# Optimization experiments

Measured on AMD Instinct MI355X. Metric: run time of the kernel, lower is better.

The kernel has to match this reference:

```python
import jax, jax.numpy as jnp
import numpy as np

B, S, D, H, F = 4, 2048, 1024, 16, 4096
BS = 64               # sparse attention block size
DH = D // H           # head dim
EPS = 1e-5


def _layer_norm(x, g, b):
    m = jnp.mean(x, axis=-1, keepdims=True)
    v = jnp.mean(jnp.square(x - m), axis=-1, keepdims=True)
    return (x - m) * jax.lax.rsqrt(v + EPS) * g + b


def setup_inputs() -> dict:
    key = jax.random.key(0)
    ks = jax.random.split(key, 12)
    sc = 0.02
    return {
        "hidden_states": jax.random.normal(ks[0], (B, S, D), dtype=jnp.float32),
        "ln1_g": jnp.ones((D,), jnp.float32), "ln1_b": jnp.zeros((D,), jnp.float32),
        "ln2_g": jnp.ones((D,), jnp.float32), "ln2_b": jnp.zeros((D,), jnp.float32),
        "wq": jax.random.normal(ks[1], (D, D), jnp.float32) * sc, "bq": jnp.zeros((D,), jnp.float32),
        "wk": jax.random.normal(ks[2], (D, D), jnp.float32) * sc, "bk": jnp.zeros((D,), jnp.float32),
        "wv": jax.random.normal(ks[3], (D, D), jnp.float32) * sc, "bv": jnp.zeros((D,), jnp.float32),
        "wo": jax.random.normal(ks[4], (D, D), jnp.float32) * sc, "bo": jnp.zeros((D,), jnp.float32),
        "w1": jax.random.normal(ks[5], (D, F), jnp.float32) * sc, "b1": jnp.zeros((F,), jnp.float32),
        "w2": jax.random.normal(ks[6], (F, D), jnp.float32) * sc, "b2": jnp.zeros((D,), jnp.float32),
    }


def _heads(x, w, b):
    # [B,S,D] -> [B,H,S/BS,BS,DH] block layout
    y = (x @ w + b).reshape(B, S, H, DH).transpose(0, 2, 1, 3)
    return y.reshape(B, H, S // BS, BS, DH)


def _block_attention(x, wq, bq, wk, bk, wv, bv, wo, bo):
    q = _heads(x, wq, bq)
    k = _heads(x, wk, bk)
    v = _heads(x, wv, bv)
    scores = jnp.einsum("bhnqd,bhnkd->bhnqk", q, k) / jnp.sqrt(jnp.float32(DH))
    w = jax.nn.softmax(scores, axis=-1)           # block-local (sparse) attention weights
    o = jnp.einsum("bhnqk,bhnkd->bhnqd", w, v)
    o = o.reshape(B, H, S, DH).transpose(0, 2, 1, 3).reshape(B, S, D)
    return o @ wo + bo, w


def reference(hidden_states, ln1_g, ln1_b, ln2_g, ln2_b,
              wq, bq, wk, bk, wv, bv, wo, bo, w1, b1, w2, b2):
    # pre-norm attention + residual
    x1 = _layer_norm(hidden_states, ln1_g, ln1_b)
    attn_out, attn_w = _block_attention(x1, wq, bq, wk, bk, wv, bv, wo, bo)
    h = hidden_states + attn_out
    # pre-norm FFN + residual (exact GELU, matching torch nn.GELU default)
    x2 = _layer_norm(h, ln2_g, ln2_b)
    ff = jax.nn.gelu(x2 @ w1 + b1, approximate=False) @ w2 + b2
    return h + ff, attn_w
```

## Files before the change

kernel.cpp:

```cpp
#include <hip/hip_runtime.h>
#include <hip/hip_bf16.h>
#include <cmath>

using bf16 = __hip_bfloat16;
typedef __attribute__((ext_vector_type(8))) short short8;
typedef __attribute__((ext_vector_type(4))) float f32x4;

#define LDK 72

__device__ __forceinline__ float bf2f(bf16 v){ return __bfloat162float(v); }
__device__ __forceinline__ bf16 f2bf(float v){ return __float2bfloat16(v); }

__device__ __forceinline__ void ld16(const void* g, void* l) {
    __builtin_amdgcn_global_load_lds(
        (const __attribute__((address_space(1))) void*)g,
        (__attribute__((address_space(3))) void*)l, 16, 0, 0);
}

__device__ __forceinline__ float gelu_f(float x) {
    float u = 0.7978845608028654f * x * (1.0f + 0.044715f * x * x);
    float e = __expf(2.0f * u);
    float t = 1.0f - 2.0f / (e + 1.0f);
    return 0.5f * x * (1.0f + t);
}

__global__ __launch_bounds__(256) void transpose_f32_bf16(
    const float* __restrict__ in, bf16* __restrict__ out, int R, int C)
{
    __shared__ __align__(16) bf16 tile[64][72];
    const int c0 = blockIdx.x * 64, r0 = blockIdx.y * 64;
    const int t = threadIdx.x;
    const int lr = t >> 3, lc = (t & 7) * 8;
    for (int p = 0; p < 2; ++p) {
        int r = p * 32 + lr;
        const float* src = in + (size_t)(r0 + r) * C + c0 + lc;
        float4 a = *(const float4*)src;
        float4 b = *(const float4*)(src + 4);
        tile[r][lc + 0] = f2bf(a.x); tile[r][lc + 1] = f2bf(a.y);
        tile[r][lc + 2] = f2bf(a.z); tile[r][lc + 3] = f2bf(a.w);
        tile[r][lc + 4] = f2bf(b.x); tile[r][lc + 5] = f2bf(b.y);
        tile[r][lc + 6] = f2bf(b.z); tile[r][lc + 7] = f2bf(b.w);
    }
    __syncthreads();
    for (int p = 0; p < 2; ++p) {
        int r = p * 32 + lr;
        short8 v;
        for (int j = 0; j < 8; ++j) v[j] = *(const short*)&tile[lc + j][r];
        *(short8*)(out + (size_t)(c0 + r) * R + r0 + lc) = v;
    }
}

__global__ __launch_bounds__(256) void concat_bias(
    const float* __restrict__ bq, const float* __restrict__ bk,
    const float* __restrict__ bv, float* __restrict__ out)
{
    int i = blockIdx.x * 256 + threadIdx.x;
    const float* src = (i < 1024) ? bq : ((i < 2048) ? bk : bv);
    out[i] = src[i & 1023];
}

__global__ __launch_bounds__(256) void layernorm_k(
    const float* __restrict__ x, const float* __restrict__ g,
    const float* __restrict__ bta, bf16* __restrict__ out)
{
    const int row = blockIdx.x, t = threadIdx.x;
    const float* xr = x + (size_t)row * 1024;
    float v[4], s1 = 0.f, s2 = 0.f;
    for (int j = 0; j < 4; ++j) {
        float f = xr[j * 256 + t];
        v[j] = f; s1 += f; s2 += f * f;
    }
    for (int d = 1; d < 64; d <<= 1) { s1 += __shfl_xor(s1, d); s2 += __shfl_xor(s2, d); }
    __shared__ float red[2][4];
    int wave = t >> 6, lane = t & 63;
    if (lane == 0) { red[0][wave] = s1; red[1][wave] = s2; }
    __syncthreads();
    s1 = red[0][0] + red[0][1] + red[0][2] + red[0][3];
    s2 = red[1][0] + red[1][1] + red[1][2] + red[1][3];
    float mean = s1 * (1.0f / 1024.0f);
    float var  = s2 * (1.0f / 1024.0f) - mean * mean;
    float rs   = rsqrtf(var + 1e-5f);
    bf16* orow = out + (size_t)row * 1024;
    for (int j = 0; j < 4; ++j) {
        int c = j * 256 + t;
        orow[c] = f2bf((v[j] - mean) * rs * g[c] + bta[c]);
    }
}

template <int MODE, int TM>
__global__ __launch_bounds__(256) void gemm_bt(
    const bf16* __restrict__ A, const bf16* __restrict__ Bt,
    const float* __restrict__ bias, const float* __restrict__ res,
    void* __restrict__ C, int M, int N, int K)
{
    constexpr int MI = TM / 32;
    __shared__ __align__(16) bf16 As0[TM * 64];
    __shared__ __align__(16) bf16 Bs0[128 * 64];
    __shared__ __align__(16) bf16 As1[TM * 64];
    __shared__ __align__(16) bf16 Bs1[128 * 64];
    const int m0 = blockIdx.x * TM, n0 = blockIdx.y * 128;
    const int t = threadIdx.x;
    const int wave = t >> 6, lane = t & 63, lhi = lane >> 4, llo = lane & 15;
    const int wm = (wave & 1) * (TM / 2), wn = (wave >> 1) * 64;
    const int lrow = lane >> 3;
    const int lcolsw = ((lane & 7) ^ lrow) * 8;

    const bf16* Ag = A  + (size_t)(m0 + lrow) * K + lcolsw;
    const bf16* Bg = Bt + (size_t)(n0 + lrow) * K + lcolsw;

    f32x4 acc[MI][4];
    for (int i = 0; i < MI; ++i)
        for (int j = 0; j < 4; ++j) acc[i][j] = (f32x4){0.f, 0.f, 0.f, 0.f};

    auto issue = [&](int k0, bf16* As, bf16* Bs) {
        for (int p = 0; p < TM / 32; ++p) {
            int rb = wave * (TM / 4) + p * 8;
            ld16(Ag + (size_t)rb * K + k0, &As[rb * 64]);
        }
        for (int p = 0; p < 4; ++p) {
            int rb = wave * 32 + p * 8;
            ld16(Bg + (size_t)rb * K + k0, &Bs[rb * 64]);
        }
    };
    auto compute = [&](const bf16* As, const bf16* Bs) {
        for (int kk = 0; kk < 64; kk += 32) {
            const int gb = kk >> 3;
            short8 af[MI], bfr[4];
            for (int i = 0; i < MI; ++i) {
                int row = wm + i * 16 + llo;
                af[i] = *(const short8*)&As[row * 64 + (((gb + lhi) ^ (llo & 7)) * 8)];
            }
            for (int i = 0; i < 4; ++i) {
                int row = wn + i * 16 + llo;
                bfr[i] = *(const short8*)&Bs[row * 64 + (((gb + lhi) ^ (llo & 7)) * 8)];
            }
            for (int mi = 0; mi < MI; ++mi)
                for (int ni = 0; ni < 4; ++ni)
                    acc[mi][ni] = __builtin_amdgcn_mfma_f32_16x16x32_bf16(
                        af[mi], bfr[ni], acc[mi][ni], 0, 0, 0);
        }
    };

    issue(0, As0, Bs0);
    for (int k0 = 0; k0 < K; k0 += 128) {
        __syncthreads();
        issue(k0 + 64, As1, Bs1);
        compute(As0, Bs0);
        __syncthreads();
        if (k0 + 128 < K) issue(k0 + 128, As0, Bs0);
        compute(As1, Bs1);
    }

    for (int mi = 0; mi < MI; ++mi)
        for (int ni = 0; ni < 4; ++ni) {
            int row = m0 + wm + mi * 16 + lhi * 4;
            int col = n0 + wn + ni * 16 + llo;
            float bcol = bias[col];
            for (int r = 0; r < 4; ++r) {
                size_t idx = (size_t)(row + r) * N + col;
                float v = acc[mi][ni][r] + bcol;
                if (MODE == 0) {
                    ((bf16*)C)[idx] = f2bf(v);
                } else if (MODE == 1) {
                    ((float*)C)[idx] = v + res[idx];
                } else if (MODE == 2) {
                    ((bf16*)C)[idx] = f2bf(gelu_f(v));
                } else {
                    ((float*)C)[idx] = v + res[idx];
                }
            }
        }
}

__global__ __launch_bounds__(256) void attn_kernel(
    const bf16* __restrict__ qkv, float* __restrict__ attw, bf16* __restrict__ o)
{
    __shared__ __align__(16) bf16 qs[64][LDK];
    __shared__ __align__(16) bf16 ks[64][LDK];
    __shared__ __align__(16) bf16 vs[64][LDK];
    const int gid = blockIdx.x;
    const int blk = gid & 31, h = (gid >> 5) & 15, b = gid >> 9;
    const int t = threadIdx.x, wave = t >> 6, lane = t & 63;
    const int lhi = lane >> 4, llo = lane & 15;
    const int srow = t >> 3, scol = (t & 7) * 8;

    for (int p = 0; p < 2; ++p) {
        int r = p * 32 + srow;
        const bf16* base = qkv + (size_t)(b * 2048 + blk * 64 + r) * 3072 + h * 64 + scol;
        *(short8*)&qs[r][scol] = *(const short8*)(base);
        *(short8*)&ks[r][scol] = *(const short8*)(base + 1024);
        *(short8*)&vs[r][scol] = *(const short8*)(base + 2048);
    }
    __syncthreads();

    f32x4 sacc[4];
    for (int j = 0; j < 4; ++j) sacc[j] = (f32x4){0.f, 0.f, 0.f, 0.f};
    for (int kk = 0; kk < 64; kk += 32) {
        short8 aq = *(const short8*)&qs[wave * 16 + llo][kk + lhi * 8];
        for (int j = 0; j < 4; ++j) {
            short8 bk = *(const short8*)&ks[j * 16 + llo][kk + lhi * 8];
            sacc[j] = __builtin_amdgcn_mfma_f32_16x16x32_bf16(aq, bk, sacc[j], 0, 0, 0);
        }
    }
    float inv[4];
    for (int r = 0; r < 4; ++r) {
        float m = -1e30f;
        for (int j = 0; j < 4; ++j) m = fmaxf(m, sacc[j][r]);
        for (int d = 1; d < 16; d <<= 1) m = fmaxf(m, __shfl_xor(m, d));
        float s = 0.f;
        for (int j = 0; j < 4; ++j) {
            float e = expf((sacc[j][r] - m) * 0.125f);
            sacc[j][r] = e; s += e;
        }
        for (int d = 1; d < 16; d <<= 1) s += __shfl_xor(s, d);
        inv[r] = 1.0f / s;
    }
    __syncthreads();
    const size_t wbase = (size_t)gid * 4096;
    for (int j = 0; j < 4; ++j)
        for (int r = 0; r < 4; ++r) {
            int row = wave * 16 + lhi * 4 + r, col = j * 16 + llo;
            float pw = sacc[j][r] * inv[r];
            qs[row][col] = f2bf(pw);
            attw[wbase + row * 64 + col] = pw;
        }
    __syncthreads();

    f32x4 oacc[4];
    for (int nt = 0; nt < 4; ++nt) oacc[nt] = (f32x4){0.f, 0.f, 0.f, 0.f};
    for (int kk = 0; kk < 64; kk += 32) {
        short8 aw = *(const short8*)&qs[wave * 16 + llo][kk + lhi * 8];
        for (int nt = 0; nt < 4; ++nt) {
            short8 bv;
            for (int jj = 0; jj < 8; ++jj)
                bv[jj] = *(const short*)&vs[kk + lhi * 8 + jj][nt * 16 + llo];
            oacc[nt] = __builtin_amdgcn_mfma_f32_16x16x32_bf16(aw, bv, oacc[nt], 0, 0, 0);
        }
    }
    for (int nt = 0; nt < 4; ++nt)
        for (int r = 0; r < 4; ++r) {
            int row = wave * 16 + lhi * 4 + r, col = nt * 16 + llo;
            o[(size_t)(b * 2048 + blk * 64 + row) * 1024 + h * 64 + col] = f2bf(oacc[nt][r]);
        }
}

extern "C" void kernel_launch(void* const* d_in, const int* in_sizes, int n_in,
                              void* d_out, int out_size, void* d_ws, size_t ws_size,
                              hipStream_t stream)
{
    const float* hidden = (const float*)d_in[0];
    const float* ln1_g  = (const float*)d_in[1];
    const float* ln1_b  = (const float*)d_in[2];
    const float* ln2_g  = (const float*)d_in[3];
    const float* ln2_b  = (const float*)d_in[4];
    const float* wq = (const float*)d_in[5];  const float* bq = (const float*)d_in[6];
    const float* wk = (const float*)d_in[7];  const float* bk = (const float*)d_in[8];
    const float* wv = (const float*)d_in[9];  const float* bv = (const float*)d_in[10];
    const float* wo = (const float*)d_in[11]; const float* bo = (const float*)d_in[12];
    const float* w1 = (const float*)d_in[13]; const float* b1 = (const float*)d_in[14];
    const float* w2 = (const float*)d_in[15]; const float* b2 = (const float*)d_in[16];

    char* ws = (char*)d_ws;
    const size_t MB = 1u << 20;
    bf16*  wqkvT   = (bf16*)(ws +  0 * MB);
    bf16*  woT     = (bf16*)(ws +  6 * MB);
    bf16*  w1T     = (bf16*)(ws +  8 * MB);
    bf16*  w2T     = (bf16*)(ws + 16 * MB);
    float* biasQKV = (float*)(ws + 24 * MB);
    bf16*  x       = (bf16*)(ws + 25 * MB);
    bf16*  qkv     = (bf16*)(ws + 41 * MB);
    float* hbuf    = (float*)(ws + 41 * MB);
    bf16*  ffc     = (bf16*)(ws + 73 * MB);
    bf16*  obuf    = (bf16*)(ws + 89 * MB);

    float* out0 = (float*)d_out;
    float* attw = (float*)d_out + (size_t)8192 * 1024;

    transpose_f32_bf16<<<dim3(16, 16), 256, 0, stream>>>(wq, wqkvT,                 1024, 1024);
    transpose_f32_bf16<<<dim3(16, 16), 256, 0, stream>>>(wk, wqkvT + 1024 * 1024,   1024, 1024);
    transpose_f32_bf16<<<dim3(16, 16), 256, 0, stream>>>(wv, wqkvT + 2*1024*1024,   1024, 1024);
    transpose_f32_bf16<<<dim3(16, 16), 256, 0, stream>>>(wo, woT, 1024, 1024);
    transpose_f32_bf16<<<dim3(64, 16), 256, 0, stream>>>(w1, w1T, 1024, 4096);
    transpose_f32_bf16<<<dim3(16, 64), 256, 0, stream>>>(w2, w2T, 4096, 1024);
    concat_bias<<<12, 256, 0, stream>>>(bq, bk, bv, biasQKV);

    layernorm_k<<<8192, 256, 0, stream>>>(hidden, ln1_g, ln1_b, x);

    gemm_bt<0, 128><<<dim3(64, 24), 256, 0, stream>>>(x, wqkvT, biasQKV, nullptr, qkv,
                                                      8192, 3072, 1024);

    attn_kernel<<<2048, 256, 0, stream>>>(qkv, attw, obuf);

    gemm_bt<1, 64><<<dim3(128, 8), 256, 0, stream>>>(obuf, woT, bo, hidden, hbuf,
                                                     8192, 1024, 1024);

    layernorm_k<<<8192, 256, 0, stream>>>(hbuf, ln2_g, ln2_b, x);

    gemm_bt<2, 128><<<dim3(64, 32), 256, 0, stream>>>(x, w1T, b1, nullptr, ffc,
                                                      8192, 4096, 1024);

    gemm_bt<3, 64><<<dim3(128, 8), 256, 0, stream>>>(ffc, w2T, b2, hbuf, out0,
                                                     8192, 1024, 4096);
}
```

Measured before the change: 472.3 us.

## Halve GEMM K-tile to 32, reswizzle LDS, raise occupancy via launch bounds

The GEMM's shared-memory stage drops from 64 to 32 along K, which halves LDS use per block and lets more blocks fit on a CU. Launch bounds now request 3 or 4 blocks per CU depending on tile height. The LDS layout switches to a new 4-group XOR swizzle, and the fragment offsets are computed once before the loop. The risk is twice as many barriers per K step, with less MFMA work per barrier to hide global-to-LDS latency, plus register pressure from the occupancy constraint.

```diff
diff --git a/kernel.cpp b/kernel.cpp
--- a/kernel.cpp
+++ b/kernel.cpp
@@ -88,66 +88,64 @@
 }
 
 template <int MODE, int TM>
-__global__ __launch_bounds__(256) void gemm_bt(
+__global__ __launch_bounds__(256, (TM == 128 ? 3 : 4)) void gemm_bt(
     const bf16* __restrict__ A, const bf16* __restrict__ Bt,
     const float* __restrict__ bias, const float* __restrict__ res,
     void* __restrict__ C, int M, int N, int K)
 {
     constexpr int MI = TM / 32;
-    __shared__ __align__(16) bf16 As0[TM * 64];
-    __shared__ __align__(16) bf16 Bs0[128 * 64];
-    __shared__ __align__(16) bf16 As1[TM * 64];
-    __shared__ __align__(16) bf16 Bs1[128 * 64];
+    constexpr int AR = TM / 64;
+    __shared__ __align__(16) bf16 As0[TM * 32];
+    __shared__ __align__(16) bf16 Bs0[128 * 32];
+    __shared__ __align__(16) bf16 As1[TM * 32];
+    __shared__ __align__(16) bf16 Bs1[128 * 32];
     const int m0 = blockIdx.x * TM, n0 = blockIdx.y * 128;
     const int t = threadIdx.x;
     const int wave = t >> 6, lane = t & 63, lhi = lane >> 4, llo = lane & 15;
     const int wm = (wave & 1) * (TM / 2), wn = (wave >> 1) * 64;
-    const int lrow = lane >> 3;
-    const int lcolsw = ((lane & 7) ^ lrow) * 8;
-
-    const bf16* Ag = A  + (size_t)(m0 + lrow) * K + lcolsw;
-    const bf16* Bg = Bt + (size_t)(n0 + lrow) * K + lcolsw;
+
+    const int srow = t >> 2;
+    const int sg   = (t & 3) ^ ((t >> 3) & 3);
+    const bf16* Asrc = A  + (size_t)(m0 + srow) * K + sg * 8;
+    const bf16* Bsrc = Bt + (size_t)(n0 + srow) * K + sg * 8;
+
+    int offA[MI], offB[4];
+    for (int i = 0; i < MI; ++i) {
+        int row = wm + i * 16 + llo;
+        offA[i] = row * 32 + (lhi ^ ((row >> 1) & 3)) * 8;
+    }
+    for (int i = 0; i < 4; ++i) {
+        int row = wn + i * 16 + llo;
+        offB[i] = row * 32 + (lhi ^ ((row >> 1) & 3)) * 8;
+    }
 
     f32x4 acc[MI][4];
     for (int i = 0; i < MI; ++i)
         for (int j = 0; j < 4; ++j) acc[i][j] = (f32x4){0.f, 0.f, 0.f, 0.f};
 
     auto issue = [&](int k0, bf16* As, bf16* Bs) {
-        for (int p = 0; p < TM / 32; ++p) {
-            int rb = wave * (TM / 4) + p * 8;
-            ld16(Ag + (size_t)rb * K + k0, &As[rb * 64]);
-        }
-        for (int p = 0; p < 4; ++p) {
-            int rb = wave * 32 + p * 8;
-            ld16(Bg + (size_t)rb * K + k0, &Bs[rb * 64]);
-        }
+        for (int p = 0; p < AR; ++p)
+            ld16(Asrc + (size_t)p * 64 * K + k0, As + p * 2048 + wave * 512);
+        for (int p = 0; p < 2; ++p)
+            ld16(Bsrc + (size_t)p * 64 * K + k0, Bs + p * 2048 + wave * 512);
     };
     auto compute = [&](const bf16* As, const bf16* Bs) {
-        for (int kk = 0; kk < 64; kk += 32) {
-            const int gb = kk >> 3;
-            short8 af[MI], bfr[4];
-            for (int i = 0; i < MI; ++i) {
-                int row = wm + i * 16 + llo;
-                af[i] = *(const short8*)&As[row * 64 + (((gb + lhi) ^ (llo & 7)) * 8)];
-            }
-            for (int i = 0; i < 4; ++i) {
-                int row = wn + i * 16 + llo;
-                bfr[i] = *(const short8*)&Bs[row * 64 + (((gb + lhi) ^ (llo & 7)) * 8)];
-            }
-            for (int mi = 0; mi < MI; ++mi)
-                for (int ni = 0; ni < 4; ++ni)
-                    acc[mi][ni] = __builtin_amdgcn_mfma_f32_16x16x32_bf16(
-                        af[mi], bfr[ni], acc[mi][ni], 0, 0, 0);
-        }
+        short8 af[MI], bfr[4];
+        for (int i = 0; i < MI; ++i) af[i]  = *(const short8*)&As[offA[i]];
+        for (int i = 0; i < 4;  ++i) bfr[i] = *(const short8*)&Bs[offB[i]];
+        for (int mi = 0; mi < MI; ++mi)
+            for (int ni = 0; ni < 4; ++ni)
+                acc[mi][ni] = __builtin_amdgcn_mfma_f32_16x16x32_bf16(
+                    af[mi], bfr[ni], acc[mi][ni], 0, 0, 0);
     };
 
     issue(0, As0, Bs0);
-    for (int k0 = 0; k0 < K; k0 += 128) {
+    for (int k0 = 0; k0 < K; k0 += 64) {
         __syncthreads();
-        issue(k0 + 64, As1, Bs1);
+        issue(k0 + 32, As1, Bs1);
         compute(As0, Bs0);
         __syncthreads();
-        if (k0 + 128 < K) issue(k0 + 128, As0, Bs0);
+        if (k0 + 64 < K) issue(k0 + 64, As0, Bs0);
         compute(As1, Bs1);
     }
 
@@ -156,8 +154,9 @@
             int row = m0 + wm + mi * 16 + lhi * 4;
             int col = n0 + wn + ni * 16 + llo;
             float bcol = bias[col];
+            size_t base = (size_t)row * N + col;
             for (int r = 0; r < 4; ++r) {
-                size_t idx = (size_t)(row + r) * N + col;
+                size_t idx = base + (size_t)r * N;
                 float v = acc[mi][ni][r] + bcol;
                 if (MODE == 0) {
                     ((bf16*)C)[idx] = f2bf(v);
```

After: 484.2 us. 1.03x slower.
